# Optimization experiments

Hardware: AMD Instinct MI355X
Metric: run time of the kernel (lower is better)

The kernel has to match this reference:

```python
import jax, jax.numpy as jnp
import numpy as np

EPS_IN = 1e-5   # InstanceNorm1d eps
EPS_DM = 1e-8   # demodulation eps


def _dcoef(weight, style):
    # rsqrt(sum_i (W[o,i]*s[b,i])^2 + eps) -> [B, out]
    return jax.lax.rsqrt(jnp.einsum('oi,bi->bo', jnp.square(weight), jnp.square(style)) + EPS_DM)


def setup_inputs() -> dict:
    key = jax.random.key(0)
    ks = jax.random.split(key, 7)
    B, S, H = 8, 1024, 1024
    lim = 1.0 / np.sqrt(H)
    u = lambda k, shp: jax.random.uniform(k, shp, jnp.float32, -lim, lim)
    return {
        'x': jax.random.normal(ks[0], (B, S, H), jnp.float32),
        'q_weight': u(ks[1], (H, H)),
        'k_weight': u(ks[2], (H, H)),
        'v_weight': u(ks[3], (H, H)),
        'w_weight': u(ks[4], (H, H)),
        'u_weight': u(ks[5], (H, H)),
        'styles': jax.random.normal(ks[6], (B, 2 * H), jnp.float32) * 0.5 + 1.0,
        'num_heads': 16,
    }


def reference(x, q_weight, k_weight, v_weight, w_weight, u_weight, styles, num_heads):
    B, S, H = x.shape
    nh = num_heads
    d = H // nh
    scale = jnp.asarray(d, x.dtype) ** -0.5

    s1 = styles[:, :H]   # modulates input hidden dim of q/k/v
    s2 = styles[:, H:]   # modulates input hidden dim of w/u and v output

    # per-sample modulation + InstanceNorm over hidden dim
    x = x * s1[:, None, :]
    mu = jnp.mean(x, axis=-1, keepdims=True)
    var = jnp.mean(jnp.square(x - mu), axis=-1, keepdims=True)
    x = (x - mu) * jax.lax.rsqrt(var + EPS_IN)

    q_dc = _dcoef(q_weight, s1)  # [B,H]
    k_dc = _dcoef(k_weight, s1)
    v_dc = _dcoef(v_weight, s1)
    w_dc = _dcoef(w_weight, s2)
    u_dc = _dcoef(u_weight, s2)

    def heads(t):  # [B,S,H] -> [B,nh,S,d]
        return t.reshape(B, S, nh, d).transpose(0, 2, 1, 3)

    q = heads(jnp.einsum('bsh,oh->bso', x, q_weight) * q_dc[:, None, :])
    k = heads(jnp.einsum('bsh,oh->bso', x, k_weight) * k_dc[:, None, :])
    v_flat = jnp.einsum('bsh,oh->bso', x, v_weight) * v_dc[:, None, :] * s2[:, None, :]
    skip = v_flat
    v = heads(v_flat)

    attn = jnp.einsum('bhqd,bhkd->bhqk', q, k) * scale
    attn = jax.nn.softmax(attn, axis=-1)
    out = jnp.einsum('bhqk,bhkd->bhqd', attn, v).transpose(0, 2, 1, 3).reshape(B, S, H)

    out = jnp.einsum('bsh,oh->bso', out, w_weight) * w_dc[:, None, :]
    skip = jnp.einsum('bsh,oh->bso', skip, u_weight) * u_dc[:, None, :]
    return out + skip
```

## Files before the change

kernel.cpp:

```cpp
#include <hip/hip_runtime.h>
#include <hip/hip_bf16.h>

#define B_ 8
#define S_ 1024
#define H_ 1024
#define NH 16
#define DH 64
#define BS (B_*S_)
#define L2E 1.44269504f

typedef unsigned short u16;
typedef __attribute__((ext_vector_type(8))) short bf16x8;
typedef __attribute__((ext_vector_type(4))) float f32x4;
typedef __attribute__((ext_vector_type(4))) u16 u16x4;

#define MFMA(a,b,c) __builtin_amdgcn_mfma_f32_16x16x32_bf16((a),(b),(c),0,0,0)

__device__ __forceinline__ u16 f2bf(float f) {
  union { float f; unsigned u; } v; v.f = f;
  unsigned r = v.u + 0x7fffu + ((v.u >> 16) & 1u);
  return (u16)(r >> 16);
}

__device__ __forceinline__ unsigned packbf2(float a, float b) {
  union { __hip_bfloat162 h; unsigned u; } v;
  v.h = __float22bfloat162_rn(float2{a, b});
  return v.u;
}

__device__ __forceinline__ void gload16(const u16* g, u16* l) {
  __builtin_amdgcn_global_load_lds(
      (const __attribute__((address_space(1))) unsigned int*)g,
      (__attribute__((address_space(3))) unsigned int*)l, 16, 0, 0);
}

__global__ __launch_bounds__(256) void dcoef_kernel(
    const float* __restrict__ qw, const float* __restrict__ kw,
    const float* __restrict__ vw, const float* __restrict__ ww,
    const float* __restrict__ uw, const float* __restrict__ styles,
    float* __restrict__ dc) {
  int bi = blockIdx.x;
  int wsel = bi >> 10;
  int o = bi & 1023;
  const float* W = (wsel == 0) ? qw : (wsel == 1) ? kw : (wsel == 2) ? vw
                   : (wsel == 3) ? ww : uw;
  int soff = (wsel < 3) ? 0 : H_;
  int tid = threadIdx.x;
  float4 w4 = *(const float4*)(W + (size_t)o * H_ + tid * 4);
  float w2x = w4.x * w4.x, w2y = w4.y * w4.y, w2z = w4.z * w4.z, w2w = w4.w * w4.w;
  float acc[8];
#pragma unroll
  for (int b = 0; b < 8; b++) {
    float4 s4 = *(const float4*)(styles + (size_t)b * 2 * H_ + soff + tid * 4);
    acc[b] = w2x * s4.x * s4.x + w2y * s4.y * s4.y + w2z * s4.z * s4.z + w2w * s4.w * s4.w;
  }
#pragma unroll
  for (int off = 1; off < 64; off <<= 1)
#pragma unroll
    for (int b = 0; b < 8; b++) acc[b] += __shfl_xor(acc[b], off);
  __shared__ float red[4][8];
  int w = tid >> 6, l = tid & 63;
  if (l == 0)
#pragma unroll
    for (int b = 0; b < 8; b++) red[w][b] = acc[b];
  __syncthreads();
  if (tid < 8) {
    int b = tid;
    float v = red[0][b] + red[1][b] + red[2][b] + red[3][b];
    float r = rsqrtf(v + 1e-8f);
    if (wsel == 2) r *= styles[(size_t)b * 2 * H_ + H_ + o];
    dc[(size_t)wsel * B_ * H_ + b * H_ + o] = r;
  }
}

__global__ __launch_bounds__(256) void wconv_kernel(
    const float* __restrict__ qw, const float* __restrict__ kw,
    const float* __restrict__ vw, const float* __restrict__ ww,
    const float* __restrict__ uw, u16* __restrict__ w16) {
  int i = blockIdx.x * 256 + threadIdx.x;
  int idx = i * 4;
  int wsel = idx >> 20;
  int off = idx & (H_ * H_ - 1);
  const float* W = (wsel == 0) ? qw : (wsel == 1) ? kw : (wsel == 2) ? vw
                   : (wsel == 3) ? ww : uw;
  float4 v = *(const float4*)(W + off);
  u16x4 o = { f2bf(v.x), f2bf(v.y), f2bf(v.z), f2bf(v.w) };
  *(u16x4*)(w16 + idx) = o;
}

__global__ __launch_bounds__(256) void ln_kernel(
    const float* __restrict__ x, const float* __restrict__ styles,
    u16* __restrict__ xn) {
  int row = blockIdx.x;
  int b = row >> 10;
  int tid = threadIdx.x;
  const float4 xv = *(const float4*)(x + (size_t)row * H_ + tid * 4);
  const float4 sv = *(const float4*)(styles + (size_t)b * 2 * H_ + tid * 4);
  float v0 = xv.x * sv.x, v1 = xv.y * sv.y, v2 = xv.z * sv.z, v3 = xv.w * sv.w;
  float sum = v0 + v1 + v2 + v3;
  float sq = v0 * v0 + v1 * v1 + v2 * v2 + v3 * v3;
#pragma unroll
  for (int off = 1; off < 64; off <<= 1) {
    sum += __shfl_xor(sum, off);
    sq += __shfl_xor(sq, off);
  }
  __shared__ float rsum[4], rsq[4];
  int w = tid >> 6;
  if ((tid & 63) == 0) { rsum[w] = sum; rsq[w] = sq; }
  __syncthreads();
  sum = rsum[0] + rsum[1] + rsum[2] + rsum[3];
  sq = rsq[0] + rsq[1] + rsq[2] + rsq[3];
  float mean = sum * (1.f / H_);
  float var = sq * (1.f / H_) - mean * mean;
  float rstd = rsqrtf(var + 1e-5f);
  u16x4 o = { f2bf((v0 - mean) * rstd), f2bf((v1 - mean) * rstd),
              f2bf((v2 - mean) * rstd), f2bf((v3 - mean) * rstd) };
  *(u16x4*)(xn + (size_t)row * H_ + tid * 4) = o;
}

__device__ __forceinline__ void stage_tile(const u16* __restrict__ src, int K,
                                           u16* dst, int srow, int schunkSw,
                                           int schunk) {
#pragma unroll
  for (int i = 0; i < 4; i++)
    gload16(src + (size_t)(srow + 32 * i) * K + schunkSw * 8,
            dst + (srow + 32 * i) * 64 + schunk * 8);
}

__device__ __forceinline__ void gemm128_bk64(
    const u16* __restrict__ Arow, const u16* __restrict__ Brow, int K, int NT,
    u16* ldsA, u16* ldsB, f32x4 acc[4][4]) {
  const int tid = threadIdx.x;
  const int l = tid & 63, w = tid >> 6;
  const int wm = (w >> 1) * 64, wn = (w & 1) * 64;
  const int lrow = l & 15, lg = l >> 4;
  const int swr = lrow & 7;
  const int srow = tid >> 3, schunk = tid & 7;
  const int schunkSw = schunk ^ (srow & 7);
  stage_tile(Arow, K, ldsA, srow, schunkSw, schunk);
  stage_tile(Brow, K, ldsB, srow, schunkSw, schunk);
  asm volatile("s_waitcnt vmcnt(0)" ::: "memory");
  __builtin_amdgcn_s_barrier();
  for (int t = 0; t < NT; ++t) {
    const int buf = (t & 1) * (128 * 64);
    if (t + 1 < NT) {
      const int nbuf = ((t + 1) & 1) * (128 * 64);
      stage_tile(Arow + (t + 1) * 64, K, ldsA + nbuf, srow, schunkSw, schunk);
      stage_tile(Brow + (t + 1) * 64, K, ldsB + nbuf, srow, schunkSw, schunk);
    }
    const u16* At = ldsA + buf;
    const u16* Bt = ldsB + buf;
#pragma unroll
    for (int ks = 0; ks < 2; ks++) {
      bf16x8 af[4], bfr[4];
#pragma unroll
      for (int i = 0; i < 4; i++)
        af[i] = *(const bf16x8*)&At[(wm + i * 16 + lrow) * 64 +
                                    (((ks * 4 + lg) ^ swr) * 8)];
#pragma unroll
      for (int i = 0; i < 4; i++)
        bfr[i] = *(const bf16x8*)&Bt[(wn + i * 16 + lrow) * 64 +
                                     (((ks * 4 + lg) ^ swr) * 8)];
      __builtin_amdgcn_s_setprio(1);
#pragma unroll
      for (int mi = 0; mi < 4; mi++)
#pragma unroll
        for (int ni = 0; ni < 4; ni++)
          acc[mi][ni] = MFMA(af[mi], bfr[ni], acc[mi][ni]);
      __builtin_amdgcn_s_setprio(0);
    }
    asm volatile("s_waitcnt vmcnt(0)" ::: "memory");
    __builtin_amdgcn_s_barrier();
  }
}

__global__ __launch_bounds__(256) void qkv_kernel(
    const u16* __restrict__ xn, const u16* __restrict__ w16,
    const float* __restrict__ dc, u16* __restrict__ Qb, u16* __restrict__ Kb,
    u16* __restrict__ VT, u16* __restrict__ vfl) {
  __shared__ u16 ldsA[2 * 128 * 64], ldsB[2 * 128 * 64];
  int bm = blockIdx.x;
  int bn = blockIdx.y;
  f32x4 acc[4][4] = {};
  gemm128_bk64(xn + (size_t)bm * 128 * H_, w16 + (size_t)bn * 128 * H_, H_, 16,
               ldsA, ldsB, acc);
  int l = threadIdx.x & 63, w = threadIdx.x >> 6;
  int wm = (w >> 1) * 64, wn = (w & 1) * 64;
  int wsel = bn >> 3;
  int col0 = (bn & 7) * 128 + wn;
  int row0 = bm * 128 + wm;
  const float* dcw = dc + (size_t)wsel * B_ * H_;
  float extra = (wsel == 0) ? 0.125f * L2E : 1.0f;
#pragma unroll
  for (int mi = 0; mi < 4; mi++) {
#pragma unroll
    for (int ni = 0; ni < 4; ni++) {
      int col = col0 + ni * 16 + (l & 15);
      int hh = col >> 6, dd = col & 63;
      int s_base = (row0 + mi * 16 + (l >> 4) * 4) & 1023;
      int b = (row0 + mi * 16 + (l >> 4) * 4) >> 10;
      float dcv = dcw[b * H_ + col] * extra;
      u16 bv[4];
#pragma unroll
      for (int rr = 0; rr < 4; rr++)
        bv[rr] = f2bf(acc[mi][ni][rr] * dcv);
      if (wsel == 0) {
#pragma unroll
        for (int rr = 0; rr < 4; rr++)
          Qb[((size_t)(b * NH + hh) * S_ + s_base + rr) * DH + dd] = bv[rr];
      } else if (wsel == 1) {
#pragma unroll
        for (int rr = 0; rr < 4; rr++)
          Kb[((size_t)(b * NH + hh) * S_ + s_base + rr) * DH + dd] = bv[rr];
      } else {
        u16x4 pv = { bv[0], bv[1], bv[2], bv[3] };
        *(u16x4*)&VT[((size_t)(b * NH + hh) * DH + dd) * S_ + s_base] = pv;
#pragma unroll
        for (int rr = 0; rr < 4; rr++)
          vfl[(size_t)(row0 + mi * 16 + (l >> 4) * 4 + rr) * H_ + col] = bv[rr];
      }
    }
  }
}

__global__ __launch_bounds__(512) void attn_kernel(
    const u16* __restrict__ Qb, const u16* __restrict__ Kb,
    const u16* __restrict__ VT, u16* __restrict__ xat) {
  __shared__ u16 ldsK[3][64 * 64];
  __shared__ u16 ldsV[3][64 * 64];
  __shared__ unsigned pls_all[8][16 * 36];
  int tid = threadIdx.x;
  int l = tid & 63, w = tid >> 6;
  int id = blockIdx.x;
  int r = id & 7, rest = id >> 3;
  int qblk = rest & 3, a = rest >> 2;
  int hl = a * 8 + r;
  int h = hl & 15, b = hl >> 4;
  int q0 = qblk * 256 + w * 32;
  const u16* Qp = Qb + ((size_t)(b * NH + h) * S_ + q0) * DH;
  const u16* Kp = Kb + (size_t)(b * NH + h) * S_ * DH;
  const u16* Vp = VT + (size_t)(b * NH + h) * DH * S_;
  unsigned* pls = pls_all[w];
  int lr = l & 15, lg = l >> 4;
  int sw = (lr & 7) << 3;
  int srow = tid >> 3, schunk = tid & 7;
  int ssw = (schunk * 8) ^ ((srow & 7) << 3);
  const u16* Ksrc = Kp + (size_t)srow * DH + ssw;
  const u16* Vsrc = Vp + (size_t)srow * S_ + ssw;
  int sdst = srow * 64 + schunk * 8;
  gload16(Ksrc, &ldsK[0][sdst]);
  gload16(Vsrc, &ldsV[0][sdst]);
  gload16(Ksrc + 64 * DH, &ldsK[1][sdst]);
  gload16(Vsrc + 64,      &ldsV[1][sdst]);
  bf16x8 qfA0 = *(const bf16x8*)(Qp + lr * 64 + lg * 8);
  bf16x8 qfA1 = *(const bf16x8*)(Qp + lr * 64 + 32 + lg * 8);
  bf16x8 qfB0 = *(const bf16x8*)(Qp + (16 + lr) * 64 + lg * 8);
  bf16x8 qfB1 = *(const bf16x8*)(Qp + (16 + lr) * 64 + 32 + lg * 8);
  f32x4 accA[4] = {}, accB[4] = {};
  float lsA = 0.f, lsB = 0.f;
  asm volatile("s_waitcnt vmcnt(2)" ::: "memory");
  __builtin_amdgcn_s_barrier();
  int cur = 0;
  for (int t = 0; t < 16; ++t) {
    if (t + 2 < 16) {
      int nb = cur + 2; if (nb >= 3) nb -= 3;
      gload16(Ksrc + (size_t)(t + 2) * 64 * DH, &ldsK[nb][sdst]);
      gload16(Vsrc + (size_t)(t + 2) * 64,      &ldsV[nb][sdst]);
    }
    const u16* Kt = &ldsK[cur][0];
    const u16* Vt = &ldsV[cur][0];
#pragma unroll
    for (int g = 0; g < 2; g++) {
      bf16x8 q0f = (g == 0) ? qfA0 : qfB0;
      bf16x8 q1f = (g == 0) ? qfA1 : qfB1;
      f32x4 st[4];
      __builtin_amdgcn_s_setprio(1);
#pragma unroll
      for (int nt = 0; nt < 4; nt++) {
        bf16x8 kf0 = *(const bf16x8*)&Kt[(nt * 16 + lr) * 64 + ((lg * 8) ^ sw)];
        bf16x8 kf1 = *(const bf16x8*)&Kt[(nt * 16 + lr) * 64 + ((32 + lg * 8) ^ sw)];
        f32x4 z = {0.f, 0.f, 0.f, 0.f};
        z = MFMA(kf0, q0f, z);
        z = MFMA(kf1, q1f, z);
        st[nt] = z;
      }
      __builtin_amdgcn_s_setprio(0);
      float rs = 0.f;
#pragma unroll
      for (int nt = 0; nt < 4; nt++)
#pragma unroll
        for (int rr = 0; rr < 4; rr++) {
          st[nt][rr] = __builtin_exp2f(st[nt][rr]);
          rs += st[nt][rr];
        }
      rs += __shfl_xor(rs, 16);
      rs += __shfl_xor(rs, 32);
      if (g == 0) lsA += rs; else lsB += rs;
      {
        unsigned* base = pls + lr * 36;
#pragma unroll
        for (int nt = 0; nt < 4; nt++) {
          uint2 pw = { packbf2(st[nt][0], st[nt][1]),
                       packbf2(st[nt][2], st[nt][3]) };
          *(uint2*)&base[nt * 8 + lg * 2] = pw;
        }
      }
      bf16x8 pb0 = *(const bf16x8*)&pls[lr * 36 + lg * 4];
      bf16x8 pb1 = *(const bf16x8*)&pls[lr * 36 + 16 + lg * 4];
      __builtin_amdgcn_s_setprio(1);
#pragma unroll
      for (int nt = 0; nt < 4; nt++) {
        bf16x8 vf0 = *(const bf16x8*)&Vt[(nt * 16 + lr) * 64 + ((lg * 8) ^ sw)];
        bf16x8 vf1 = *(const bf16x8*)&Vt[(nt * 16 + lr) * 64 + ((32 + lg * 8) ^ sw)];
        if (g == 0) {
          accA[nt] = MFMA(vf0, pb0, accA[nt]);
          accA[nt] = MFMA(vf1, pb1, accA[nt]);
        } else {
          accB[nt] = MFMA(vf0, pb0, accB[nt]);
          accB[nt] = MFMA(vf1, pb1, accB[nt]);
        }
      }
      __builtin_amdgcn_s_setprio(0);
    }
    if (t < 14) {
      asm volatile("s_waitcnt vmcnt(2)" ::: "memory");
    } else if (t == 14) {
      asm volatile("s_waitcnt vmcnt(0)" ::: "memory");
    }
    if (t < 15) __builtin_amdgcn_s_barrier();
    cur = (cur == 2) ? 0 : cur + 1;
  }
  float invA = 1.f / lsA, invB = 1.f / lsB;
#pragma unroll
  for (int nt = 0; nt < 4; nt++) {
    u16x4 oA = { f2bf(accA[nt][0] * invA), f2bf(accA[nt][1] * invA),
                 f2bf(accA[nt][2] * invA), f2bf(accA[nt][3] * invA) };
    *(u16x4*)(xat + ((size_t)(b * S_) + q0 + lr) * H_ + h * DH + nt * 16 + lg * 4) = oA;
    u16x4 oB = { f2bf(accB[nt][0] * invB), f2bf(accB[nt][1] * invB),
                 f2bf(accB[nt][2] * invB), f2bf(accB[nt][3] * invB) };
    *(u16x4*)(xat + ((size_t)(b * S_) + q0 + 16 + lr) * H_ + h * DH + nt * 16 + lg * 4) = oB;
  }
}

__global__ __launch_bounds__(256) void out_kernel(
    const u16* __restrict__ xat, const u16* __restrict__ vfl,
    const u16* __restrict__ w16, const float* __restrict__ dc,
    float* __restrict__ out) {
  __shared__ u16 ldsA[2 * 128 * 64], ldsB[2 * 128 * 64];
  int bm = blockIdx.x;
  int bn = blockIdx.y;
  f32x4 acc[4][4] = {};
  gemm128_bk64(xat + (size_t)bm * 128 * H_,
               w16 + (size_t)3 * H_ * H_ + (size_t)bn * 128 * H_, H_, 16,
               ldsA, ldsB, acc);
  int l = threadIdx.x & 63, w = threadIdx.x >> 6;
  int wm = (w >> 1) * 64, wn = (w & 1) * 64;
  int col0 = bn * 128 + wn;
  int row0 = bm * 128 + wm;
  int b = row0 >> 10;
  const float* wdc = dc + (size_t)3 * B_ * H_ + b * H_;
  const float* udc = dc + (size_t)4 * B_ * H_ + b * H_;
  float ratio[4], ud[4];
#pragma unroll
  for (int ni = 0; ni < 4; ni++) {
    int col = col0 + ni * 16 + (l & 15);
    ud[ni] = udc[col];
    ratio[ni] = wdc[col] / ud[ni];
  }
#pragma unroll
  for (int mi = 0; mi < 4; mi++)
#pragma unroll
    for (int ni = 0; ni < 4; ni++)
#pragma unroll
      for (int rr = 0; rr < 4; rr++) acc[mi][ni][rr] *= ratio[ni];
  gemm128_bk64(vfl + (size_t)bm * 128 * H_,
               w16 + (size_t)4 * H_ * H_ + (size_t)bn * 128 * H_, H_, 16,
               ldsA, ldsB, acc);
#pragma unroll
  for (int mi = 0; mi < 4; mi++)
#pragma unroll
    for (int ni = 0; ni < 4; ni++) {
      int col = col0 + ni * 16 + (l & 15);
#pragma unroll
      for (int rr = 0; rr < 4; rr++) {
        int row = row0 + mi * 16 + (l >> 4) * 4 + rr;
        out[(size_t)row * H_ + col] = acc[mi][ni][rr] * ud[ni];
      }
    }
}

extern "C" void kernel_launch(void* const* d_in, const int* in_sizes, int n_in,
                              void* d_out, int out_size, void* d_ws, size_t ws_size,
                              hipStream_t stream) {
  const float* x = (const float*)d_in[0];
  const float* qw = (const float*)d_in[1];
  const float* kw = (const float*)d_in[2];
  const float* vw = (const float*)d_in[3];
  const float* ww = (const float*)d_in[4];
  const float* uw = (const float*)d_in[5];
  const float* styles = (const float*)d_in[6];
  float* out = (float*)d_out;

  char* ws = (char*)d_ws;
  size_t need = 163840 + (size_t)5 * H_ * H_ * 2 + (size_t)6 * BS * H_ * 2;
  if (ws_size < need) return;
  float* dc = (float*)ws;
  u16* w16 = (u16*)(ws + 163840);
  u16* xn  = w16 + (size_t)5 * H_ * H_;
  u16* Qb  = xn + (size_t)BS * H_;
  u16* Kb  = Qb + (size_t)BS * H_;
  u16* VT  = Kb + (size_t)BS * H_;
  u16* vfl = VT + (size_t)BS * H_;
  u16* xat = vfl + (size_t)BS * H_;

  dcoef_kernel<<<dim3(5 * H_), dim3(256), 0, stream>>>(qw, kw, vw, ww, uw, styles, dc);
  wconv_kernel<<<dim3(5120), dim3(256), 0, stream>>>(qw, kw, vw, ww, uw, w16);
  ln_kernel<<<dim3(BS), dim3(256), 0, stream>>>(x, styles, xn);
  qkv_kernel<<<dim3(64, 24), dim3(256), 0, stream>>>(xn, w16, dc, Qb, Kb, VT, vfl);
  attn_kernel<<<dim3(512), dim3(512), 0, stream>>>(Qb, Kb, VT, xat);
  out_kernel<<<dim3(64, 8), dim3(256), 0, stream>>>(xat, vfl, w16, dc, out);
}
```

Baseline: 204.2 us.

## Use triple-buffered BK=32 GEMM pipeline with block swizzle in projection kernels

Replaces the double-buffered BK=64 GEMM mainloop with a three-stage BK=32 pipeline. Loads are issued two tiles ahead and only partially waited on via vmcnt. LDS per block shrinks from 64KB to 48KB and launch bounds request 3 blocks per CU to raise occupancy. Block IDs are flattened and remapped with an XCD-style swizzle (bid&7) to improve L2 locality. The tradeoff is twice as many barriers per K loop and a more complex swizzled LDS indexing scheme.

```diff
diff --git a/kernel.cpp b/kernel.cpp
--- a/kernel.cpp
+++ b/kernel.cpp
@@ -118,72 +118,81 @@
   *(u16x4*)(xn + (size_t)row * H_ + tid * 4) = o;
 }
 
-__device__ __forceinline__ void stage_tile(const u16* __restrict__ src, int K,
-                                           u16* dst, int srow, int schunkSw,
-                                           int schunk) {
-#pragma unroll
-  for (int i = 0; i < 4; i++)
-    gload16(src + (size_t)(srow + 32 * i) * K + schunkSw * 8,
-            dst + (srow + 32 * i) * 64 + schunk * 8);
-}
-
-__device__ __forceinline__ void gemm128_bk64(
-    const u16* __restrict__ Arow, const u16* __restrict__ Brow, int K, int NT,
+__device__ __forceinline__ void stage32(const u16* __restrict__ src, int K,
+                                        u16* dst, int tid) {
+#pragma unroll
+  for (int i = 0; i < 2; i++) {
+    int lrow = i * 32 + (tid >> 3);
+    int ch = tid & 7;
+    int lch = ch ^ (lrow & 7);
+    int grow = lrow * 2 + (lch >> 2);
+    gload16(src + (size_t)grow * K + (lch & 3) * 8, dst + lrow * 64 + ch * 8);
+  }
+}
+
+__device__ __forceinline__ void gemm128_p3(
+    const u16* __restrict__ A, const u16* __restrict__ B, int K, int NT,
     u16* ldsA, u16* ldsB, f32x4 acc[4][4]) {
   const int tid = threadIdx.x;
   const int l = tid & 63, w = tid >> 6;
   const int wm = (w >> 1) * 64, wn = (w & 1) * 64;
-  const int lrow = l & 15, lg = l >> 4;
-  const int swr = lrow & 7;
-  const int srow = tid >> 3, schunk = tid & 7;
-  const int schunkSw = schunk ^ (srow & 7);
-  stage_tile(Arow, K, ldsA, srow, schunkSw, schunk);
-  stage_tile(Brow, K, ldsB, srow, schunkSw, schunk);
-  asm volatile("s_waitcnt vmcnt(0)" ::: "memory");
+  const int lrow = l & 15, kc = l >> 4;
+  stage32(A, K, ldsA, tid);
+  stage32(B, K, ldsB, tid);
+  stage32(A + 32, K, ldsA + 64 * 64, tid);
+  stage32(B + 32, K, ldsB + 64 * 64, tid);
+  asm volatile("s_waitcnt vmcnt(4)" ::: "memory");
   __builtin_amdgcn_s_barrier();
+  int bufc = 0;
   for (int t = 0; t < NT; ++t) {
-    const int buf = (t & 1) * (128 * 64);
-    if (t + 1 < NT) {
-      const int nbuf = ((t + 1) & 1) * (128 * 64);
-      stage_tile(Arow + (t + 1) * 64, K, ldsA + nbuf, srow, schunkSw, schunk);
-      stage_tile(Brow + (t + 1) * 64, K, ldsB + nbuf, srow, schunkSw, schunk);
-    }
-    const u16* At = ldsA + buf;
-    const u16* Bt = ldsB + buf;
-#pragma unroll
-    for (int ks = 0; ks < 2; ks++) {
-      bf16x8 af[4], bfr[4];
-#pragma unroll
-      for (int i = 0; i < 4; i++)
-        af[i] = *(const bf16x8*)&At[(wm + i * 16 + lrow) * 64 +
-                                    (((ks * 4 + lg) ^ swr) * 8)];
-#pragma unroll
-      for (int i = 0; i < 4; i++)
-        bfr[i] = *(const bf16x8*)&Bt[(wn + i * 16 + lrow) * 64 +
-                                     (((ks * 4 + lg) ^ swr) * 8)];
-      __builtin_amdgcn_s_setprio(1);
-#pragma unroll
-      for (int mi = 0; mi < 4; mi++)
-#pragma unroll
-        for (int ni = 0; ni < 4; ni++)
-          acc[mi][ni] = MFMA(af[mi], bfr[ni], acc[mi][ni]);
-      __builtin_amdgcn_s_setprio(0);
-    }
-    asm volatile("s_waitcnt vmcnt(0)" ::: "memory");
+    if (t + 2 < NT) {
+      int nb = bufc + 2; if (nb >= 3) nb -= 3;
+      stage32(A + (size_t)(t + 2) * 32, K, ldsA + nb * (64 * 64), tid);
+      stage32(B + (size_t)(t + 2) * 32, K, ldsB + nb * (64 * 64), tid);
+    }
+    const u16* At = ldsA + bufc * (64 * 64);
+    const u16* Bt = ldsB + bufc * (64 * 64);
+    bf16x8 af[4], bfr[4];
+#pragma unroll
+    for (int i = 0; i < 4; i++) {
+      int x = wm + i * 16 + lrow;
+      int ch = (((x & 1) << 2) | kc) ^ ((x >> 1) & 7);
+      af[i] = *(const bf16x8*)&At[(x >> 1) * 64 + ch * 8];
+    }
+#pragma unroll
+    for (int i = 0; i < 4; i++) {
+      int x = wn + i * 16 + lrow;
+      int ch = (((x & 1) << 2) | kc) ^ ((x >> 1) & 7);
+      bfr[i] = *(const bf16x8*)&Bt[(x >> 1) * 64 + ch * 8];
+    }
+    __builtin_amdgcn_s_setprio(1);
+#pragma unroll
+    for (int mi = 0; mi < 4; mi++)
+#pragma unroll
+      for (int ni = 0; ni < 4; ni++)
+        acc[mi][ni] = MFMA(af[mi], bfr[ni], acc[mi][ni]);
+    __builtin_amdgcn_s_setprio(0);
+    if (t + 2 < NT) {
+      asm volatile("s_waitcnt vmcnt(4)" ::: "memory");
+    } else if (t + 1 < NT) {
+      asm volatile("s_waitcnt vmcnt(0)" ::: "memory");
+    }
     __builtin_amdgcn_s_barrier();
-  }
-}
-
-__global__ __launch_bounds__(256) void qkv_kernel(
+    bufc = (bufc == 2) ? 0 : bufc + 1;
+  }
+}
+
+__global__ __launch_bounds__(256, 3) void qkv_kernel(
     const u16* __restrict__ xn, const u16* __restrict__ w16,
     const float* __restrict__ dc, u16* __restrict__ Qb, u16* __restrict__ Kb,
     u16* __restrict__ VT, u16* __restrict__ vfl) {
-  __shared__ u16 ldsA[2 * 128 * 64], ldsB[2 * 128 * 64];
-  int bm = blockIdx.x;
-  int bn = blockIdx.y;
+  __shared__ u16 ldsA[3 * 64 * 64], ldsB[3 * 64 * 64];
+  int bid = blockIdx.x;
+  int swz = (bid & 7) * 192 + (bid >> 3);
+  int bm = swz / 24, bn = swz % 24;
   f32x4 acc[4][4] = {};
-  gemm128_bk64(xn + (size_t)bm * 128 * H_, w16 + (size_t)bn * 128 * H_, H_, 16,
-               ldsA, ldsB, acc);
+  gemm128_p3(xn + (size_t)bm * 128 * H_, w16 + (size_t)bn * 128 * H_, H_, 32,
+             ldsA, ldsB, acc);
   int l = threadIdx.x & 63, w = threadIdx.x >> 6;
   int wm = (w >> 1) * 64, wn = (w & 1) * 64;
   int wsel = bn >> 3;
@@ -342,17 +351,18 @@
   }
 }
 
-__global__ __launch_bounds__(256) void out_kernel(
+__global__ __launch_bounds__(256, 3) void out_kernel(
     const u16* __restrict__ xat, const u16* __restrict__ vfl,
     const u16* __restrict__ w16, const float* __restrict__ dc,
     float* __restrict__ out) {
-  __shared__ u16 ldsA[2 * 128 * 64], ldsB[2 * 128 * 64];
-  int bm = blockIdx.x;
-  int bn = blockIdx.y;
+  __shared__ u16 ldsA[3 * 64 * 64], ldsB[3 * 64 * 64];
+  int bid = blockIdx.x;
+  int swz = (bid & 7) * 64 + (bid >> 3);
+  int bm = swz >> 3, bn = swz & 7;
   f32x4 acc[4][4] = {};
-  gemm128_bk64(xat + (size_t)bm * 128 * H_,
-               w16 + (size_t)3 * H_ * H_ + (size_t)bn * 128 * H_, H_, 16,
-               ldsA, ldsB, acc);
+  gemm128_p3(xat + (size_t)bm * 128 * H_,
+             w16 + (size_t)3 * H_ * H_ + (size_t)bn * 128 * H_, H_, 32,
+             ldsA, ldsB, acc);
   int l = threadIdx.x & 63, w = threadIdx.x >> 6;
   int wm = (w >> 1) * 64, wn = (w & 1) * 64;
   int col0 = bn * 128 + wn;
@@ -373,9 +383,9 @@
     for (int ni = 0; ni < 4; ni++)
 #pragma unroll
       for (int rr = 0; rr < 4; rr++) acc[mi][ni][rr] *= ratio[ni];
-  gemm128_bk64(vfl + (size_t)bm * 128 * H_,
-               w16 + (size_t)4 * H_ * H_ + (size_t)bn * 128 * H_, H_, 16,
-               ldsA, ldsB, acc);
+  gemm128_p3(vfl + (size_t)bm * 128 * H_,
+             w16 + (size_t)4 * H_ * H_ + (size_t)bn * 128 * H_, H_, 32,
+             ldsA, ldsB, acc);
 #pragma unroll
   for (int mi = 0; mi < 4; mi++)
 #pragma unroll
@@ -416,7 +426,7 @@
   dcoef_kernel<<<dim3(5 * H_), dim3(256), 0, stream>>>(qw, kw, vw, ww, uw, styles, dc);
   wconv_kernel<<<dim3(5120), dim3(256), 0, stream>>>(qw, kw, vw, ww, uw, w16);
   ln_kernel<<<dim3(BS), dim3(256), 0, stream>>>(x, styles, xn);
-  qkv_kernel<<<dim3(64, 24), dim3(256), 0, stream>>>(xn, w16, dc, Qb, Kb, VT, vfl);
+  qkv_kernel<<<dim3(1536), dim3(256), 0, stream>>>(xn, w16, dc, Qb, Kb, VT, vfl);
   attn_kernel<<<dim3(512), dim3(512), 0, stream>>>(Qb, Kb, VT, xat);
-  out_kernel<<<dim3(64, 8), dim3(256), 0, stream>>>(xat, vfl, w16, dc, out);
-}
+  out_kernel<<<dim3(512), dim3(256), 0, stream>>>(xat, vfl, w16, dc, out);
+}
```

Result: slower. 210.1 us (+2.9%).
